# Kernel optimization log

Hardware: AMD Instinct MI355X
Metric: run time of the kernel (lower is better)

The kernel has to match this reference:

```python
import jax, jax.numpy as jnp
import numpy as np

D_MODEL = 1024
N_HEADS = 16
D_HEAD = D_MODEL // N_HEADS
D_FF = 4096
B, L = 4, 2048


def setup_inputs() -> dict:
    key = jax.random.key(0)
    ks = jax.random.split(key, 12)
    s = 0.02
    return {
        "x": jax.random.normal(ks[0], (B, L, D_MODEL), dtype=jnp.float32),
        "ln1_g": jnp.ones((D_MODEL,), jnp.float32),
        "ln1_b": jnp.zeros((D_MODEL,), jnp.float32),
        "w_qkv": jax.random.normal(ks[1], (D_MODEL, 3 * D_MODEL), jnp.float32) * s,
        "b_qkv": jnp.zeros((3 * D_MODEL,), jnp.float32),
        "w_out": jax.random.normal(ks[2], (D_MODEL, D_MODEL), jnp.float32) * s,
        "b_out": jnp.zeros((D_MODEL,), jnp.float32),
        "ln2_g": jnp.ones((D_MODEL,), jnp.float32),
        "ln2_b": jnp.zeros((D_MODEL,), jnp.float32),
        "w1": jax.random.normal(ks[3], (D_MODEL, D_FF), jnp.float32) * s,
        "b1": jnp.zeros((D_FF,), jnp.float32),
        "w2": jax.random.normal(ks[4], (D_FF, D_MODEL), jnp.float32) * s,
        "b2": jnp.zeros((D_MODEL,), jnp.float32),
    }


def _layernorm(x, g, b, eps=1e-5):
    mu = jnp.mean(x, axis=-1, keepdims=True)
    var = jnp.var(x, axis=-1, keepdims=True)
    return (x - mu) * jax.lax.rsqrt(var + eps) * g + b


def _attention(h, w_qkv, b_qkv, w_out, b_out):
    Bx, Lx, D = h.shape
    qkv = h @ w_qkv + b_qkv  # [B,L,3D]
    qkv = qkv.reshape(Bx, Lx, 3, N_HEADS, D_HEAD)
    q, k, v = qkv[:, :, 0], qkv[:, :, 1], qkv[:, :, 2]  # [B,L,H,Dh]
    att = jnp.einsum("bqhd,bkhd->bhqk", q, k) * (D_HEAD ** -0.5)
    causal = jnp.tril(jnp.ones((Lx, Lx), bool))
    att = jnp.where(causal, att, -jnp.inf)
    att = jax.nn.softmax(att, axis=-1)
    out = jnp.einsum("bhqk,bkhd->bqhd", att, v).reshape(Bx, Lx, D)
    return out @ w_out + b_out


def reference(x, ln1_g, ln1_b, w_qkv, b_qkv, w_out, b_out,
              ln2_g, ln2_b, w1, b1, w2, b2):
    h = x + _attention(_layernorm(x, ln1_g, ln1_b), w_qkv, b_qkv, w_out, b_out)
    ff = jax.nn.gelu(_layernorm(h, ln2_g, ln2_b) @ w1 + b1, approximate=False) @ w2 + b2
    return h + ff
```

## Files before the change

### kernel.cpp

```cpp
#include <hip/hip_runtime.h>
#include <hip/hip_bf16.h>


typedef float f32x4 __attribute__((ext_vector_type(4)));
typedef __bf16 bf16x8 __attribute__((ext_vector_type(8)));
typedef unsigned short u16;

#define MFMA16(a, b, c) __builtin_amdgcn_mfma_f32_16x16x32_bf16((a), (b), (c), 0, 0, 0)

#define GLL16(g, l)                                                            \
  __builtin_amdgcn_global_load_lds(                                            \
      (__attribute__((address_space(1))) void*)(g),                            \
      (__attribute__((address_space(3))) void*)(l), 16, 0, 0)

__device__ __forceinline__ u16 f2bf(float f) {
  union { float f; unsigned int u; } x; x.f = f;
  unsigned int r = x.u + 0x7fffu + ((x.u >> 16) & 1u);
  return (u16)(r >> 16);
}

__global__ __launch_bounds__(256) void prep_kernel(
    const float* __restrict__ w_qkv, u16* __restrict__ wqkvT,
    const float* __restrict__ w_out, u16* __restrict__ woutT,
    const float* __restrict__ w1,    u16* __restrict__ w1T,
    const float* __restrict__ w2,    u16* __restrict__ w2T,
    const float* __restrict__ x, const float* __restrict__ g,
    const float* __restrict__ b, u16* __restrict__ y)
{
  __shared__ u16 tile[32][33];
  __shared__ float red[8];
  int bid = blockIdx.x;
  int t = threadIdx.x;
  if (bid < 12288) {
    const float* W; u16* Wt; int K, N, nb, base;
    if (bid < 3072)      { W = w_qkv; Wt = wqkvT; K = 1024; N = 3072; nb = 96;  base = 0; }
    else if (bid < 4096) { W = w_out; Wt = woutT; K = 1024; N = 1024; nb = 32;  base = 3072; }
    else if (bid < 8192) { W = w1;    Wt = w1T;   K = 1024; N = 4096; nb = 128; base = 4096; }
    else                 { W = w2;    Wt = w2T;   K = 4096; N = 1024; nb = 32;  base = 8192; }
    int idx = bid - base;
    int n0 = (idx % nb) * 32, k0 = (idx / nb) * 32;
    int tr = t >> 5, tc = t & 31;
#pragma unroll
    for (int i = 0; i < 4; ++i) {
      int k = k0 + tr + i * 8;
      tile[tc][tr + i * 8] = f2bf(W[(size_t)k * N + n0 + tc]);
    }
    __syncthreads();
#pragma unroll
    for (int i = 0; i < 4; ++i) {
      int n = n0 + tr + i * 8;
      Wt[(size_t)n * K + k0 + tc] = tile[tr + i * 8][tc];
    }
  } else {
    int row = bid - 12288;
    const float4* xr = (const float4*)(x + (size_t)row * 1024);
    float4 v = xr[t];
    float s  = v.x + v.y + v.z + v.w;
    float ss = v.x*v.x + v.y*v.y + v.z*v.z + v.w*v.w;
#pragma unroll
    for (int off = 1; off < 64; off <<= 1) {
      s  += __shfl_xor(s, off);
      ss += __shfl_xor(ss, off);
    }
    int w = t >> 6;
    if ((t & 63) == 0) { red[w*2] = s; red[w*2+1] = ss; }
    __syncthreads();
    s  = red[0] + red[2] + red[4] + red[6];
    ss = red[1] + red[3] + red[5] + red[7];
    float mu  = s * (1.0f / 1024.0f);
    float var = ss * (1.0f / 1024.0f) - mu * mu;
    float rs  = rsqrtf(var + 1e-5f);
    float4 gg = ((const float4*)g)[t];
    float4 bb = ((const float4*)b)[t];
    ushort4 o;
    o.x = f2bf((v.x - mu) * rs * gg.x + bb.x);
    o.y = f2bf((v.y - mu) * rs * gg.y + bb.y);
    o.z = f2bf((v.z - mu) * rs * gg.z + bb.z);
    o.w = f2bf((v.w - mu) * rs * gg.w + bb.w);
    ((ushort4*)y)[(size_t)row * 256 + t] = o;
  }
}

__global__ __launch_bounds__(256) void ln_kernel(
    const float* __restrict__ x, const float* __restrict__ g,
    const float* __restrict__ b, u16* __restrict__ y)
{
  int row = blockIdx.x;
  int t = threadIdx.x;
  const float4* xr = (const float4*)(x + (size_t)row * 1024);
  float4 v = xr[t];
  float s  = v.x + v.y + v.z + v.w;
  float ss = v.x*v.x + v.y*v.y + v.z*v.z + v.w*v.w;
#pragma unroll
  for (int off = 1; off < 64; off <<= 1) {
    s  += __shfl_xor(s, off);
    ss += __shfl_xor(ss, off);
  }
  __shared__ float red[8];
  int w = t >> 6;
  if ((t & 63) == 0) { red[w*2] = s; red[w*2+1] = ss; }
  __syncthreads();
  s  = red[0] + red[2] + red[4] + red[6];
  ss = red[1] + red[3] + red[5] + red[7];
  float mu  = s * (1.0f / 1024.0f);
  float var = ss * (1.0f / 1024.0f) - mu * mu;
  float rs  = rsqrtf(var + 1e-5f);
  float4 gg = ((const float4*)g)[t];
  float4 bb = ((const float4*)b)[t];
  ushort4 o;
  o.x = f2bf((v.x - mu) * rs * gg.x + bb.x);
  o.y = f2bf((v.y - mu) * rs * gg.y + bb.y);
  o.z = f2bf((v.z - mu) * rs * gg.z + bb.z);
  o.w = f2bf((v.w - mu) * rs * gg.w + bb.w);
  ((ushort4*)y)[(size_t)row * 256 + t] = o;
}

template<int GELU, int HAS_RES, int OUT_BF16>
__global__ __launch_bounds__(256, 2) void gemm_kernel(
    const u16* __restrict__ A, const u16* __restrict__ Bt,
    const float* __restrict__ bias, const float* __restrict__ res,
    void* __restrict__ Cout, int M, int N, int K)
{
  __shared__ u16 lA[2][128 * 32];
  __shared__ u16 lB[2][128 * 32];
  const int nbn = N >> 7;
  int nwg = gridDim.x;
  int wg = blockIdx.x;
  if ((nwg & 7) == 0) wg = (wg & 7) * (nwg >> 3) + (wg >> 3);
  int bm = wg / nbn, bn = wg % nbn;
  int tid = threadIdx.x;
  int w = tid >> 6, l = tid & 63;
  int lh = l & 15, lg = l >> 4;
  int wr = w >> 1, wc = w & 1;
  const size_t Kb = (size_t)K * 2;
  const char* Ab = (const char*)A + (size_t)(bm * 128) * Kb;
  const char* Bb = (const char*)Bt + (size_t)(bn * 128) * Kb;

  int c0 = w * 64 + l;
  int r0 = c0 >> 2, sw0 = ((c0 ^ (c0 >> 3)) & 3) << 4;
  int c1 = (4 + w) * 64 + l;
  int r1 = c1 >> 2, sw1 = ((c1 ^ (c1 >> 3)) & 3) << 4;

#define GSTAGE(sel, kt)                                                        \
  do {                                                                         \
    GLL16(Ab + (size_t)r0 * Kb + (size_t)(kt) * 64 + sw0,                      \
          (char*)lA[sel] + w * 1024);                                          \
    GLL16(Bb + (size_t)r0 * Kb + (size_t)(kt) * 64 + sw0,                      \
          (char*)lB[sel] + w * 1024);                                          \
    GLL16(Ab + (size_t)r1 * Kb + (size_t)(kt) * 64 + sw1,                      \
          (char*)lA[sel] + (4 + w) * 1024);                                    \
    GLL16(Bb + (size_t)r1 * Kb + (size_t)(kt) * 64 + sw1,                      \
          (char*)lB[sel] + (4 + w) * 1024);                                    \
  } while (0)

  const int swo = ((lg ^ (lh >> 1)) & 3) << 4;
  const int offA = (wr * 64 + lh) * 64 + swo;
  const int offB = (wc * 64 + lh) * 64 + swo;

  f32x4 acc[4][4] = {};
  const int nkt = K >> 5;
  GSTAGE(0, 0);
  __syncthreads();
  int cur = 0;
#pragma unroll 1
  for (int kt = 0; kt < nkt; ++kt) {
    if (kt + 1 < nkt) GSTAGE(cur ^ 1, kt + 1);
    const char* bufA = (const char*)lA[cur];
    const char* bufB = (const char*)lB[cur];
    bf16x8 af[4], bfr[4];
#pragma unroll
    for (int m = 0; m < 4; ++m)
      af[m] = *(const bf16x8*)(bufA + offA + m * 1024);
#pragma unroll
    for (int n = 0; n < 4; ++n)
      bfr[n] = *(const bf16x8*)(bufB + offB + n * 1024);
#pragma unroll
    for (int m = 0; m < 4; ++m)
#pragma unroll
      for (int n = 0; n < 4; ++n)
        acc[m][n] = MFMA16(af[m], bfr[n], acc[m][n]);
    __syncthreads();
    cur ^= 1;
  }
#undef GSTAGE

#pragma unroll
  for (int m = 0; m < 4; ++m) {
    int row0 = bm * 128 + wr * 64 + m * 16 + lg * 4;
#pragma unroll
    for (int n = 0; n < 4; ++n) {
      int col = bn * 128 + wc * 64 + n * 16 + lh;
      float bv = bias[col];
#pragma unroll
      for (int r = 0; r < 4; ++r) {
        int row = row0 + r;
        float v = acc[m][n][r] + bv;
        if (GELU) v = 0.5f * v * (1.0f + erff(v * 0.70710678118f));
        if (HAS_RES) v += res[(size_t)row * N + col];
        if (OUT_BF16) ((u16*)Cout)[(size_t)row * N + col] = f2bf(v);
        else ((float*)Cout)[(size_t)row * N + col] = v;
      }
    }
  }
  (void)M;
}

template<int GELU, int HAS_RES, int OUT_BF16, int VT_FUSE>
__global__ __launch_bounds__(256, 2) void gemm_ring3(
    const u16* __restrict__ A, const u16* __restrict__ Bt,
    const float* __restrict__ bias, const float* __restrict__ res,
    void* __restrict__ Cout, u16* __restrict__ vt, int M, int N, int K)
{
  __shared__ u16 lA[3][128 * 32];
  __shared__ u16 lB[3][128 * 32];
  const int nbn = N >> 7;
  int nwg = gridDim.x;
  int wg = blockIdx.x;
  if ((nwg & 7) == 0) wg = (wg & 7) * (nwg >> 3) + (wg >> 3);
  int bm = wg / nbn, bn = wg % nbn;
  int tid = threadIdx.x;
  int w = tid >> 6, l = tid & 63;
  int lh = l & 15, lg = l >> 4;
  int wr = w >> 1, wc = w & 1;
  const size_t Kb = (size_t)K * 2;
  const char* Ab = (const char*)A + (size_t)(bm * 128) * Kb;
  const char* Bb = (const char*)Bt + (size_t)(bn * 128) * Kb;

  int c0 = w * 64 + l;
  int r0 = c0 >> 2, sw0 = ((c0 ^ (c0 >> 3)) & 3) << 4;
  int c1 = (4 + w) * 64 + l;
  int r1 = c1 >> 2, sw1 = ((c1 ^ (c1 >> 3)) & 3) << 4;

#define GSTAGE(sel, kt)                                                        \
  do {                                                                         \
    GLL16(Ab + (size_t)r0 * Kb + (size_t)(kt) * 64 + sw0,                      \
          (char*)lA[sel] + w * 1024);                                          \
    GLL16(Bb + (size_t)r0 * Kb + (size_t)(kt) * 64 + sw0,                      \
          (char*)lB[sel] + w * 1024);                                          \
    GLL16(Ab + (size_t)r1 * Kb + (size_t)(kt) * 64 + sw1,                      \
          (char*)lA[sel] + (4 + w) * 1024);                                    \
    GLL16(Bb + (size_t)r1 * Kb + (size_t)(kt) * 64 + sw1,                      \
          (char*)lB[sel] + (4 + w) * 1024);                                    \
  } while (0)

  const int swo = ((lg ^ (lh >> 1)) & 3) << 4;
  const int offA = (wr * 64 + lh) * 64 + swo;
  const int offB = (wc * 64 + lh) * 64 + swo;

  f32x4 acc[4][4] = {};
  const int nkt = K >> 5;
  GSTAGE(0, 0);
  GSTAGE(1, 1);
  asm volatile("s_waitcnt vmcnt(4)" ::: "memory");
  __builtin_amdgcn_s_barrier();
  __builtin_amdgcn_sched_barrier(0);

  int cur = 0, s2 = 2;
#pragma unroll 1
  for (int t = 0; t < nkt; ++t) {
    const char* bufA = (const char*)lA[cur];
    const char* bufB = (const char*)lB[cur];
    bf16x8 af[4], bfr[4];
#pragma unroll
    for (int m = 0; m < 4; ++m)
      af[m] = *(const bf16x8*)(bufA + offA + m * 1024);
#pragma unroll
    for (int n = 0; n < 4; ++n)
      bfr[n] = *(const bf16x8*)(bufB + offB + n * 1024);
    if (t + 2 < nkt) GSTAGE(s2, t + 2);
    __builtin_amdgcn_s_setprio(1);
#pragma unroll
    for (int m = 0; m < 4; ++m)
#pragma unroll
      for (int n = 0; n < 4; ++n)
        acc[m][n] = MFMA16(af[m], bfr[n], acc[m][n]);
    __builtin_amdgcn_s_setprio(0);
    if (t < nkt - 1) {
      __builtin_amdgcn_sched_barrier(0);
      if (t < nkt - 2) asm volatile("s_waitcnt vmcnt(4)" ::: "memory");
      else             asm volatile("s_waitcnt vmcnt(0)" ::: "memory");
      __builtin_amdgcn_s_barrier();
      __builtin_amdgcn_sched_barrier(0);
    }
    cur = (cur == 2) ? 0 : cur + 1;
    s2  = (s2 == 2) ? 0 : s2 + 1;
  }
#undef GSTAGE

#pragma unroll
  for (int m = 0; m < 4; ++m) {
    int row0 = bm * 128 + wr * 64 + m * 16 + lg * 4;
#pragma unroll
    for (int n = 0; n < 4; ++n) {
      int col = bn * 128 + wc * 64 + n * 16 + lh;
      float bv = bias[col];
      if (VT_FUSE && col >= 2048) {
        int hh = (col - 2048) >> 6, dd = (col - 2048) & 63;
        int bb = row0 >> 11, ll = row0 & 2047;
        ushort4 pk;
        pk.x = f2bf(acc[m][n][0] + bv);
        pk.y = f2bf(acc[m][n][1] + bv);
        pk.z = f2bf(acc[m][n][2] + bv);
        pk.w = f2bf(acc[m][n][3] + bv);
        *(ushort4*)(vt + ((size_t)((bb * 16 + hh) * 64 + dd)) * 2048 + ll) = pk;
      } else {
#pragma unroll
        for (int r = 0; r < 4; ++r) {
          int row = row0 + r;
          float v = acc[m][n][r] + bv;
          if (GELU) v = 0.5f * v * (1.0f + erff(v * 0.70710678118f));
          if (HAS_RES) v += res[(size_t)row * N + col];
          if (OUT_BF16) ((u16*)Cout)[(size_t)row * N + col] = f2bf(v);
          else ((float*)Cout)[(size_t)row * N + col] = v;
        }
      }
    }
  }
  (void)M;
}

__global__ __launch_bounds__(256, 4) void attn_kernel(
    const u16* __restrict__ qkv, const u16* __restrict__ vt,
    u16* __restrict__ out)
{
  __shared__ u16 Ks[2][4096];
  __shared__ u16 Vs[2][4096];
  __shared__ u16 Ps[4][1024];

  const float C = 0.18033688011f;

  int bid = blockIdx.x;
  int pi = bid >> 6, bh = bid & 63;
  int b = bh >> 4, h = bh & 15;
  int tid = threadIdx.x;
  int w = tid >> 6, l = tid & 63;
  int lh = l & 15, lg = l >> 4;
  int lh7 = lh & 7;

  const char* kg = (const char*)qkv + (size_t)(b * 2048) * 6144 + 2048 + h * 128;
  const char* vg = (const char*)vt + (size_t)((b * 16 + h) * 64) * 4096;
  char* pbw = (char*)Ps[w] + lh * 128;

#pragma unroll 1
  for (int half = 0; half < 2; ++half) {
    int qb = half ? (31 - pi) : pi;
    int q0 = qb * 64 + w * 16;
    const u16* qbase = qkv + ((size_t)(b * 2048) + q0) * 3072 + h * 64;
    bf16x8 aq0 = *(const bf16x8*)(qbase + (size_t)lh * 3072 + lg * 8);
    bf16x8 aq1 = *(const bf16x8*)(qbase + (size_t)lh * 3072 + 32 + lg * 8);

    f32x4 o[4] = {};
    float m = -1e30f;
    float lsum = 0.f;
    int nt = qb + 1;

    __syncthreads();
#pragma unroll
    for (int i = 0; i < 2; ++i) {
      int u = tid + i * 256;
      int row = u >> 3, uc = u & 7, sw = uc ^ (row & 7);
      GLL16(kg + (size_t)row * 6144 + sw * 16,
            (char*)Ks[0] + (size_t)(i * 256 + w * 64) * 16);
      GLL16(vg + (size_t)row * 4096 + sw * 16,
            (char*)Vs[0] + (size_t)(i * 256 + w * 64) * 16);
    }

#pragma unroll 1
    for (int kt = 0; kt < nt; ++kt) {
      int cur = kt & 1;
      __syncthreads();
      if (kt + 1 < nt) {
        int nxt = cur ^ 1;
        size_t kofs = (size_t)(kt + 1) * 64;
#pragma unroll
        for (int i = 0; i < 2; ++i) {
          int u = tid + i * 256;
          int row = u >> 3, uc = u & 7, sw = uc ^ (row & 7);
          GLL16(kg + (kofs + row) * 6144 + sw * 16,
                (char*)Ks[nxt] + (size_t)(i * 256 + w * 64) * 16);
          GLL16(vg + (size_t)row * 4096 + kofs * 2 + sw * 16,
                (char*)Vs[nxt] + (size_t)(i * 256 + w * 64) * 16);
        }
      }
      const char* kbuf = (const char*)Ks[cur];
      f32x4 s[4];
      __builtin_amdgcn_s_setprio(1);
#pragma unroll
      for (int kb = 0; kb < 4; ++kb) {
        int row = kb * 16 + lh;
        const char* rp = kbuf + row * 128;
        bf16x8 a0 = *(const bf16x8*)(rp + ((lg ^ lh7) << 4));
        bf16x8 a1 = *(const bf16x8*)(rp + (((4 + lg) ^ lh7) << 4));
        f32x4 z = {0.f, 0.f, 0.f, 0.f};
        z = MFMA16(a0, aq0, z);
        z = MFMA16(a1, aq1, z);
        s[kb] = z;
      }
      __builtin_amdgcn_s_setprio(0);
      if (kt == qb) {
        int qin = w * 16 + lh;
#pragma unroll
        for (int kb = 0; kb < 4; ++kb)
#pragma unroll
          for (int r = 0; r < 4; ++r)
            if (kb * 16 + lg * 4 + r > qin) s[kb][r] = -1e30f;
      }
      float tm = fmaxf(fmaxf(s[0][0], s[0][1]), fmaxf(s[0][2], s[0][3]));
#pragma unroll
      for (int kb = 1; kb < 4; ++kb)
        tm = fmaxf(tm, fmaxf(fmaxf(s[kb][0], s[kb][1]), fmaxf(s[kb][2], s[kb][3])));
      tm = fmaxf(tm, __shfl_xor(tm, 16));
      tm = fmaxf(tm, __shfl_xor(tm, 32));
      if (__any(tm > m + 64.0f)) {
        float nm = fmaxf(m, tm);
        float f = __builtin_amdgcn_exp2f((m - nm) * C);
        m = nm; lsum *= f;
#pragma unroll
        for (int db = 0; db < 4; ++db)
#pragma unroll
          for (int r = 0; r < 4; ++r) o[db][r] *= f;
      }
      float mc = m * C;
      float ps = 0.f;
#pragma unroll
      for (int kb = 0; kb < 4; ++kb)
#pragma unroll
        for (int r = 0; r < 4; ++r) {
          float p = __builtin_amdgcn_exp2f(fmaf(s[kb][r], C, -mc));
          s[kb][r] = p;
          ps += p;
        }
      ps += __shfl_xor(ps, 16);
      ps += __shfl_xor(ps, 32);
      lsum += ps;
#pragma unroll
      for (int kb = 0; kb < 4; ++kb) {
        unsigned lo, hi;
        asm("v_cvt_pk_bf16_f32 %0, %1, %2" : "=v"(lo) : "v"(s[kb][0]), "v"(s[kb][1]));
        asm("v_cvt_pk_bf16_f32 %0, %1, %2" : "=v"(hi) : "v"(s[kb][2]), "v"(s[kb][3]));
        int unit = kb * 2 + (lg >> 1);
        uint2 val; val.x = lo; val.y = hi;
        *(uint2*)(pbw + ((unit ^ lh7) << 4) + ((lg & 1) << 3)) = val;
      }
      bf16x8 pa0 = *(const bf16x8*)(pbw + ((lg ^ lh7) << 4));
      bf16x8 pa1 = *(const bf16x8*)(pbw + (((4 + lg) ^ lh7) << 4));
      const char* vbuf = (const char*)Vs[cur];
      __builtin_amdgcn_s_setprio(1);
#pragma unroll
      for (int db = 0; db < 4; ++db) {
        int row = db * 16 + lh;
        const char* rp = vbuf + row * 128;
        bf16x8 v0 = *(const bf16x8*)(rp + ((lg ^ lh7) << 4));
        bf16x8 v1 = *(const bf16x8*)(rp + (((4 + lg) ^ lh7) << 4));
        o[db] = MFMA16(v0, pa0, o[db]);
        o[db] = MFMA16(v1, pa1, o[db]);
      }
      __builtin_amdgcn_s_setprio(0);
    }
    float rinv = 1.0f / lsum;
    u16* ob = out + ((size_t)(b * 2048) + q0 + lh) * 1024 + h * 64;
#pragma unroll
    for (int db = 0; db < 4; ++db) {
      ushort4 pk;
      pk.x = f2bf(o[db][0] * rinv);
      pk.y = f2bf(o[db][1] * rinv);
      pk.z = f2bf(o[db][2] * rinv);
      pk.w = f2bf(o[db][3] * rinv);
      *(ushort4*)(ob + db * 16 + lg * 4) = pk;
    }
  }
}

extern "C" void kernel_launch(void* const* d_in, const int* in_sizes, int n_in,
                              void* d_out, int out_size, void* d_ws, size_t ws_size,
                              hipStream_t stream) {
  const float* x     = (const float*)d_in[0];
  const float* ln1_g = (const float*)d_in[1];
  const float* ln1_b = (const float*)d_in[2];
  const float* w_qkv = (const float*)d_in[3];
  const float* b_qkv = (const float*)d_in[4];
  const float* w_out = (const float*)d_in[5];
  const float* b_out = (const float*)d_in[6];
  const float* ln2_g = (const float*)d_in[7];
  const float* ln2_b = (const float*)d_in[8];
  const float* w1    = (const float*)d_in[9];
  const float* b1    = (const float*)d_in[10];
  const float* w2    = (const float*)d_in[11];
  const float* b2    = (const float*)d_in[12];

  char* ws = (char*)d_ws;
  u16* wqkvT = (u16*)(ws + 0);
  u16* woutT = (u16*)(ws + 6291456);
  u16* w1T   = (u16*)(ws + 8388608);
  u16* w2T   = (u16*)(ws + 16777216);
  u16* qkv   = (u16*)(ws + 25165824);
  u16* ffn1  = (u16*)(ws + 25165824);
  u16* vtb   = (u16*)(ws + 75497472);
  u16* lnb   = (u16*)(ws + 92274688);
  u16* attn  = lnb;
  float* h   = (float*)(ws + 125829120);

  prep_kernel<<<20480, 256, 0, stream>>>(w_qkv, wqkvT, w_out, woutT,
                                         w1, w1T, w2, w2T,
                                         x, ln1_g, ln1_b, lnb);
  gemm_ring3<0, 0, 1, 1><<<1536, 256, 0, stream>>>(lnb, wqkvT, b_qkv, nullptr, qkv, vtb, 8192, 3072, 1024);
  attn_kernel<<<1024, 256, 0, stream>>>(qkv, vtb, attn);
  gemm_ring3<0, 1, 0, 0><<<512, 256, 0, stream>>>(attn, woutT, b_out, x, h, nullptr, 8192, 1024, 1024);
  ln_kernel<<<8192, 256, 0, stream>>>(h, ln2_g, ln2_b, lnb);
  gemm_kernel<1, 0, 1><<<2048, 256, 0, stream>>>(lnb, w1T, b1, nullptr, ffn1, 8192, 4096, 1024);
  gemm_ring3<0, 1, 0, 0><<<512, 256, 0, stream>>>(ffn1, w2T, b2, h, (float*)d_out, nullptr, 8192, 1024, 4096);
}
```

Baseline: 369.8 us.

## Share K/V tile loads between paired query blocks in causal attention

```diff
diff --git a/kernel.cpp b/kernel.cpp
--- a/kernel.cpp
+++ b/kernel.cpp
@@ -341,48 +341,48 @@
   const char* vg = (const char*)vt + (size_t)((b * 16 + h) * 64) * 4096;
   char* pbw = (char*)Ps[w] + lh * 128;
 
+  const int qbA = pi, qbB = 31 - pi;
+  const int q0A = qbA * 64 + w * 16, q0B = qbB * 64 + w * 16;
+  const u16* qApt = qkv + ((size_t)(b * 2048) + q0A) * 3072 + h * 64;
+  const u16* qBpt = qkv + ((size_t)(b * 2048) + q0B) * 3072 + h * 64;
+  bf16x8 aqB0 = *(const bf16x8*)(qBpt + (size_t)lh * 3072 + lg * 8);
+  bf16x8 aqB1 = *(const bf16x8*)(qBpt + (size_t)lh * 3072 + 32 + lg * 8);
+
+  f32x4 oA[4] = {}, oB[4] = {};
+  float mA = -1e30f, lsA = 0.f, mB = -1e30f, lsB = 0.f;
+  const int nt = qbB + 1;
+
+#pragma unroll
+  for (int i = 0; i < 2; ++i) {
+    int u = tid + i * 256;
+    int row = u >> 3, uc = u & 7, sw = uc ^ (row & 7);
+    GLL16(kg + (size_t)row * 6144 + sw * 16,
+          (char*)Ks[0] + (size_t)(i * 256 + w * 64) * 16);
+    GLL16(vg + (size_t)row * 4096 + sw * 16,
+          (char*)Vs[0] + (size_t)(i * 256 + w * 64) * 16);
+  }
+
 #pragma unroll 1
-  for (int half = 0; half < 2; ++half) {
-    int qb = half ? (31 - pi) : pi;
-    int q0 = qb * 64 + w * 16;
-    const u16* qbase = qkv + ((size_t)(b * 2048) + q0) * 3072 + h * 64;
-    bf16x8 aq0 = *(const bf16x8*)(qbase + (size_t)lh * 3072 + lg * 8);
-    bf16x8 aq1 = *(const bf16x8*)(qbase + (size_t)lh * 3072 + 32 + lg * 8);
-
-    f32x4 o[4] = {};
-    float m = -1e30f;
-    float lsum = 0.f;
-    int nt = qb + 1;
-
+  for (int kt = 0; kt < nt; ++kt) {
+    int cur = kt & 1;
     __syncthreads();
-#pragma unroll
-    for (int i = 0; i < 2; ++i) {
-      int u = tid + i * 256;
-      int row = u >> 3, uc = u & 7, sw = uc ^ (row & 7);
-      GLL16(kg + (size_t)row * 6144 + sw * 16,
-            (char*)Ks[0] + (size_t)(i * 256 + w * 64) * 16);
-      GLL16(vg + (size_t)row * 4096 + sw * 16,
-            (char*)Vs[0] + (size_t)(i * 256 + w * 64) * 16);
-    }
-
-#pragma unroll 1
-    for (int kt = 0; kt < nt; ++kt) {
-      int cur = kt & 1;
-      __syncthreads();
-      if (kt + 1 < nt) {
-        int nxt = cur ^ 1;
-        size_t kofs = (size_t)(kt + 1) * 64;
-#pragma unroll
-        for (int i = 0; i < 2; ++i) {
-          int u = tid + i * 256;
-          int row = u >> 3, uc = u & 7, sw = uc ^ (row & 7);
-          GLL16(kg + (kofs + row) * 6144 + sw * 16,
-                (char*)Ks[nxt] + (size_t)(i * 256 + w * 64) * 16);
-          GLL16(vg + (size_t)row * 4096 + kofs * 2 + sw * 16,
-                (char*)Vs[nxt] + (size_t)(i * 256 + w * 64) * 16);
-        }
-      }
-      const char* kbuf = (const char*)Ks[cur];
+    if (kt + 1 < nt) {
+      int nxt = cur ^ 1;
+      size_t kofs = (size_t)(kt + 1) * 64;
+#pragma unroll
+      for (int i = 0; i < 2; ++i) {
+        int u = tid + i * 256;
+        int row = u >> 3, uc = u & 7, sw = uc ^ (row & 7);
+        GLL16(kg + (kofs + row) * 6144 + sw * 16,
+              (char*)Ks[nxt] + (size_t)(i * 256 + w * 64) * 16);
+        GLL16(vg + (size_t)row * 4096 + kofs * 2 + sw * 16,
+              (char*)Vs[nxt] + (size_t)(i * 256 + w * 64) * 16);
+      }
+    }
+    const char* kbuf = (const char*)Ks[cur];
+    const char* vbuf = (const char*)Vs[cur];
+
+    {
       f32x4 s[4];
       __builtin_amdgcn_s_setprio(1);
 #pragma unroll
@@ -392,12 +392,12 @@
         bf16x8 a0 = *(const bf16x8*)(rp + ((lg ^ lh7) << 4));
         bf16x8 a1 = *(const bf16x8*)(rp + (((4 + lg) ^ lh7) << 4));
         f32x4 z = {0.f, 0.f, 0.f, 0.f};
-        z = MFMA16(a0, aq0, z);
-        z = MFMA16(a1, aq1, z);
+        z = MFMA16(a0, aqB0, z);
+        z = MFMA16(a1, aqB1, z);
         s[kb] = z;
       }
       __builtin_amdgcn_s_setprio(0);
-      if (kt == qb) {
+      if (kt == qbB) {
         int qin = w * 16 + lh;
 #pragma unroll
         for (int kb = 0; kb < 4; ++kb)
@@ -411,16 +411,16 @@
         tm = fmaxf(tm, fmaxf(fmaxf(s[kb][0], s[kb][1]), fmaxf(s[kb][2], s[kb][3])));
       tm = fmaxf(tm, __shfl_xor(tm, 16));
       tm = fmaxf(tm, __shfl_xor(tm, 32));
-      if (__any(tm > m + 64.0f)) {
-        float nm = fmaxf(m, tm);
-        float f = __builtin_amdgcn_exp2f((m - nm) * C);
-        m = nm; lsum *= f;
+      if (__any(tm > mB + 64.0f)) {
+        float nm = fmaxf(mB, tm);
+        float f = __builtin_amdgcn_exp2f((mB - nm) * C);
+        mB = nm; lsB *= f;
 #pragma unroll
         for (int db = 0; db < 4; ++db)
 #pragma unroll
-          for (int r = 0; r < 4; ++r) o[db][r] *= f;
-      }
-      float mc = m * C;
+          for (int r = 0; r < 4; ++r) oB[db][r] *= f;
+      }
+      float mc = mB * C;
       float ps = 0.f;
 #pragma unroll
       for (int kb = 0; kb < 4; ++kb)
@@ -432,7 +432,7 @@
         }
       ps += __shfl_xor(ps, 16);
       ps += __shfl_xor(ps, 32);
-      lsum += ps;
+      lsB += ps;
 #pragma unroll
       for (int kb = 0; kb < 4; ++kb) {
         unsigned lo, hi;
@@ -444,7 +444,6 @@
       }
       bf16x8 pa0 = *(const bf16x8*)(pbw + ((lg ^ lh7) << 4));
       bf16x8 pa1 = *(const bf16x8*)(pbw + (((4 + lg) ^ lh7) << 4));
-      const char* vbuf = (const char*)Vs[cur];
       __builtin_amdgcn_s_setprio(1);
 #pragma unroll
       for (int db = 0; db < 4; ++db) {
@@ -452,20 +451,113 @@
         const char* rp = vbuf + row * 128;
         bf16x8 v0 = *(const bf16x8*)(rp + ((lg ^ lh7) << 4));
         bf16x8 v1 = *(const bf16x8*)(rp + (((4 + lg) ^ lh7) << 4));
-        o[db] = MFMA16(v0, pa0, o[db]);
-        o[db] = MFMA16(v1, pa1, o[db]);
+        oB[db] = MFMA16(v0, pa0, oB[db]);
+        oB[db] = MFMA16(v1, pa1, oB[db]);
       }
       __builtin_amdgcn_s_setprio(0);
     }
-    float rinv = 1.0f / lsum;
-    u16* ob = out + ((size_t)(b * 2048) + q0 + lh) * 1024 + h * 64;
+
+    if (kt <= qbA) {
+      bf16x8 aqA0 = *(const bf16x8*)(qApt + (size_t)lh * 3072 + lg * 8);
+      bf16x8 aqA1 = *(const bf16x8*)(qApt + (size_t)lh * 3072 + 32 + lg * 8);
+      f32x4 s[4];
+      __builtin_amdgcn_s_setprio(1);
+#pragma unroll
+      for (int kb = 0; kb < 4; ++kb) {
+        int row = kb * 16 + lh;
+        const char* rp = kbuf + row * 128;
+        bf16x8 a0 = *(const bf16x8*)(rp + ((lg ^ lh7) << 4));
+        bf16x8 a1 = *(const bf16x8*)(rp + (((4 + lg) ^ lh7) << 4));
+        f32x4 z = {0.f, 0.f, 0.f, 0.f};
+        z = MFMA16(a0, aqA0, z);
+        z = MFMA16(a1, aqA1, z);
+        s[kb] = z;
+      }
+      __builtin_amdgcn_s_setprio(0);
+      if (kt == qbA) {
+        int qin = w * 16 + lh;
+#pragma unroll
+        for (int kb = 0; kb < 4; ++kb)
+#pragma unroll
+          for (int r = 0; r < 4; ++r)
+            if (kb * 16 + lg * 4 + r > qin) s[kb][r] = -1e30f;
+      }
+      float tm = fmaxf(fmaxf(s[0][0], s[0][1]), fmaxf(s[0][2], s[0][3]));
+#pragma unroll
+      for (int kb = 1; kb < 4; ++kb)
+        tm = fmaxf(tm, fmaxf(fmaxf(s[kb][0], s[kb][1]), fmaxf(s[kb][2], s[kb][3])));
+      tm = fmaxf(tm, __shfl_xor(tm, 16));
+      tm = fmaxf(tm, __shfl_xor(tm, 32));
+      if (__any(tm > mA + 64.0f)) {
+        float nm = fmaxf(mA, tm);
+        float f = __builtin_amdgcn_exp2f((mA - nm) * C);
+        mA = nm; lsA *= f;
+#pragma unroll
+        for (int db = 0; db < 4; ++db)
+#pragma unroll
+          for (int r = 0; r < 4; ++r) oA[db][r] *= f;
+      }
+      float mc = mA * C;
+      float ps = 0.f;
+#pragma unroll
+      for (int kb = 0; kb < 4; ++kb)
+#pragma unroll
+        for (int r = 0; r < 4; ++r) {
+          float p = __builtin_amdgcn_exp2f(fmaf(s[kb][r], C, -mc));
+          s[kb][r] = p;
+          ps += p;
+        }
+      ps += __shfl_xor(ps, 16);
+      ps += __shfl_xor(ps, 32);
+      lsA += ps;
+#pragma unroll
+      for (int kb = 0; kb < 4; ++kb) {
+        unsigned lo, hi;
+        asm("v_cvt_pk_bf16_f32 %0, %1, %2" : "=v"(lo) : "v"(s[kb][0]), "v"(s[kb][1]));
+        asm("v_cvt_pk_bf16_f32 %0, %1, %2" : "=v"(hi) : "v"(s[kb][2]), "v"(s[kb][3]));
+        int unit = kb * 2 + (lg >> 1);
+        uint2 val; val.x = lo; val.y = hi;
+        *(uint2*)(pbw + ((unit ^ lh7) << 4) + ((lg & 1) << 3)) = val;
+      }
+      bf16x8 pa0 = *(const bf16x8*)(pbw + ((lg ^ lh7) << 4));
+      bf16x8 pa1 = *(const bf16x8*)(pbw + (((4 + lg) ^ lh7) << 4));
+      __builtin_amdgcn_s_setprio(1);
+#pragma unroll
+      for (int db = 0; db < 4; ++db) {
+        int row = db * 16 + lh;
+        const char* rp = vbuf + row * 128;
+        bf16x8 v0 = *(const bf16x8*)(rp + ((lg ^ lh7) << 4));
+        bf16x8 v1 = *(const bf16x8*)(rp + (((4 + lg) ^ lh7) << 4));
+        oA[db] = MFMA16(v0, pa0, oA[db]);
+        oA[db] = MFMA16(v1, pa1, oA[db]);
+      }
+      __builtin_amdgcn_s_setprio(0);
+    }
+  }
+
+  {
+    float rinv = 1.0f / lsB;
+    u16* ob = out + ((size_t)(b * 2048) + q0B + lh) * 1024 + h * 64;
 #pragma unroll
     for (int db = 0; db < 4; ++db) {
       ushort4 pk;
-      pk.x = f2bf(o[db][0] * rinv);
-      pk.y = f2bf(o[db][1] * rinv);
-      pk.z = f2bf(o[db][2] * rinv);
-      pk.w = f2bf(o[db][3] * rinv);
+      pk.x = f2bf(oB[db][0] * rinv);
+      pk.y = f2bf(oB[db][1] * rinv);
+      pk.z = f2bf(oB[db][2] * rinv);
+      pk.w = f2bf(oB[db][3] * rinv);
+      *(ushort4*)(ob + db * 16 + lg * 4) = pk;
+    }
+  }
+  {
+    float rinv = 1.0f / lsA;
+    u16* ob = out + ((size_t)(b * 2048) + q0A + lh) * 1024 + h * 64;
+#pragma unroll
+    for (int db = 0; db < 4; ++db) {
+      ushort4 pk;
+      pk.x = f2bf(oA[db][0] * rinv);
+      pk.y = f2bf(oA[db][1] * rinv);
+      pk.z = f2bf(oA[db][2] * rinv);
+      pk.w = f2bf(oA[db][3] * rinv);
       *(ushort4*)(ob + db * 16 + lg * 4) = pk;
     }
   }
```

New measurement: 367.2 us. Within noise of the previous version (-0.7%).
